# Optimization experiments

Hardware: AMD Instinct MI355X
Metric: run time of the kernel (lower is better)

## Reference

```python
import jax, jax.numpy as jnp
import numpy as np

HIDDEN = 4096
FFN = 14336
GS = 64  # groupsize


def dequant2(qw, scales, zeros, N):
    """Unpack 2-bit HQQ weights. qw: (N//4, K) int32, scales/zeros: (G, K).
    Returns W of shape (N, K) float: (bits - zeros[n % G]) * scales[n % G]."""
    G = scales.shape[0]
    n = jnp.arange(N)
    packed = qw[n // 4]                      # (N, K)
    shift = ((3 - (n % 4)) * 2).astype(qw.dtype)  # per-row bit shift
    vals = (packed >> shift[:, None]) & 3    # (N, K) 2-bit codes
    g = n % G
    return (vals.astype(scales.dtype) - zeros[g]) * scales[g]


def setup_inputs() -> dict:
    key = jax.random.key(0)
    ks = jax.random.split(key, 12)
    x = jax.random.normal(ks[0], (512, HIDDEN), dtype=jnp.float32)
    qw1 = jax.random.randint(ks[1], (FFN // 4, HIDDEN), 0, 256, dtype=jnp.int32)
    qw3 = jax.random.randint(ks[2], (FFN // 4, HIDDEN), 0, 256, dtype=jnp.int32)
    qw2 = jax.random.randint(ks[3], (HIDDEN // 4, FFN), 0, 256, dtype=jnp.int32)
    G1 = FFN // GS
    G2 = HIDDEN // GS
    s1 = jax.random.uniform(ks[4], (G1, HIDDEN), dtype=jnp.float32) * 0.05
    z1 = jax.random.uniform(ks[5], (G1, HIDDEN), dtype=jnp.float32)
    s3 = jax.random.uniform(ks[6], (G1, HIDDEN), dtype=jnp.float32) * 0.05
    z3 = jax.random.uniform(ks[7], (G1, HIDDEN), dtype=jnp.float32)
    s2 = jax.random.uniform(ks[8], (G2, FFN), dtype=jnp.float32) * 0.05
    z2 = jax.random.uniform(ks[9], (G2, FFN), dtype=jnp.float32)
    return {"x": x, "qw1": qw1, "s1": s1, "z1": z1, "qw3": qw3, "s3": s3,
            "z3": z3, "qw2": qw2, "s2": s2, "z2": z2, "groupsize": GS}


def reference(x, qw1, s1, z1, qw3, s3, z3, qw2, s2, z2, groupsize):
    # gate / up projections: C = x @ W^T, W dequantized to (N, K)
    w1 = dequant2(qw1, s1, z1, FFN)      # (FFN, HIDDEN)
    w3 = dequant2(qw3, s3, z3, FFN)      # (FFN, HIDDEN)
    w2 = dequant2(qw2, s2, z2, HIDDEN)   # (HIDDEN, FFN)
    gate = jnp.einsum('mk,nk->mn', x, w1)   # (M, FFN)
    up = jnp.einsum('mk,nk->mn', x, w3)     # (M, FFN)
    h = jax.nn.silu(gate) * up               # SwiGLU
    out = jnp.einsum('mf,hf->mh', h, w2)     # (M, HIDDEN)
    return out
```

## Files before the change

### kernel.cpp

```cpp
#include <hip/hip_runtime.h>
#include <hip/hip_fp16.h>
#include <stdint.h>

#define HIDDEN 4096
#define FFN    14336
#define MDIM   512
#define G1     224
#define G2     64
#define BK     64
#define KB_H   128
#define KB_F   448

typedef _Float16 f16x8 __attribute__((ext_vector_type(8)));
typedef float f32x4 __attribute__((ext_vector_type(4)));

#define SCHED0() __builtin_amdgcn_sched_barrier(0);
#define LGKM_BAR()                                            \
    asm volatile("s_waitcnt lgkmcnt(0)" ::: "memory");        \
    __builtin_amdgcn_s_barrier();                             \
    __builtin_amdgcn_sched_barrier(0);


__global__ void cvt_xp_kernel(const float* __restrict__ x, ushort* __restrict__ xbp) {
    int i = blockIdx.x * blockDim.x + threadIdx.x;
    int ls = i & 63;
    int kb = (i >> 6) & (KB_H - 1);
    int mb = i >> 13;
    int row = mb * 16 + (ls & 15);
    int col = kb * 32 + (ls >> 4) * 8;
    const float4* src = (const float4*)&x[(size_t)row * HIDDEN + col];
    float4 v0 = src[0], v1 = src[1];
    __half2 h0 = __floats2half2_rn(v0.x, v0.y);
    __half2 h1 = __floats2half2_rn(v0.z, v0.w);
    __half2 h2 = __floats2half2_rn(v1.x, v1.y);
    __half2 h3 = __floats2half2_rn(v1.z, v1.w);
    uint4 o = make_uint4(__builtin_bit_cast(uint32_t, h0), __builtin_bit_cast(uint32_t, h1),
                         __builtin_bit_cast(uint32_t, h2), __builtin_bit_cast(uint32_t, h3));
    ((uint4*)xbp)[i] = o;
}

__global__ void build_sz_kernel(const float* __restrict__ s, const float* __restrict__ z,
                                uint32_t* __restrict__ outp) {
    int i = blockIdx.x * blockDim.x + threadIdx.x;
    float s0 = s[2 * i], s1 = s[2 * i + 1];
    float z0 = z[2 * i], z1 = z[2 * i + 1];
    __half2 hs = __floats2half2_rn(s0, s1);
    __half2 hn = __floats2half2_rn(-z0 * s0, -z1 * s1);
    ((uint2*)outp)[i] = make_uint2(__builtin_bit_cast(uint32_t, hs),
                                   __builtin_bit_cast(uint32_t, hn));
}

__device__ __forceinline__ uint32_t deq2(uint32_t w0, uint32_t w1, uint32_t sh,
                                         uint32_t spair, uint32_t npair) {
    uint32_t c0 = (w0 >> sh) & 3u;
    uint32_t c1 = (w1 >> sh) & 3u;
    uint32_t sel = 0x01000100u + c0 * 0x0202u + c1 * 0x02020000u;
    uint32_t codes = __builtin_amdgcn_perm(0x42004000u, 0x3C000000u, sel);
    __half2 r = __hfma2(__builtin_bit_cast(__half2, codes),
                        __builtin_bit_cast(__half2, spair),
                        __builtin_bit_cast(__half2, npair));
    return __builtin_bit_cast(uint32_t, r);
}


__global__ __launch_bounds__(256, 3)
void gemm_gateup(const ushort* __restrict__ xbp, const uint32_t* __restrict__ qw1,
                 const uint32_t* __restrict__ sz1, const uint32_t* __restrict__ qw3,
                 const uint32_t* __restrict__ sz3, ushort* __restrict__ hp) {
    __shared__ ushort sB1[2][32 * 64];
    __shared__ ushort sB2[2][32 * 64];
    __shared__ ushort sE[256 * 32];

    const int tid = threadIdx.x;
    const int idx = ((blockIdx.x & 7) * 112) + (blockIdx.x >> 3);
    const int mt = idx & 1, nt = idx >> 1;
    const int m0 = mt * 256, n0 = nt * 32;

    const int lane = tid & 63, w = tid >> 6;
    const int wm = w * 64;
    const int frow = lane & 15, fk = (lane >> 4) * 8;
    const int sw = (frow & 7) << 3;

    uint32_t abase[4];
#pragma unroll
    for (int mi = 0; mi < 4; ++mi)
        abase[mi] = (uint32_t)(((m0 >> 4) + w * 4 + mi) * KB_H) * 512 + lane * 8;

    const int bi = tid & 127;
    const int rp = bi >> 3;
    const int kc = (bi & 7) * 8;
    const int row0 = rp * 2;
    const int g0 = (n0 + row0) % G1;
    const uint32_t* qp = (tid < 128 ? qw1 : qw3) + (size_t)(n0 / 4 + (rp >> 1)) * HIDDEN + kc;
    const uint32_t* zp = (tid < 128 ? sz1 : sz3) + (size_t)g0 * HIDDEN + kc;
    ushort (*sB)[32 * 64] = (tid < 128) ? sB1 : sB2;
    const uint32_t sh0 = 6u - 4u * (uint32_t)(rp & 1);
    const int wc0 = row0 * 64 + (kc ^ ((row0 & 7) << 3));
    const int wc1 = (row0 + 1) * 64 + (kc ^ (((row0 + 1) & 7) << 3));

    f32x4 accG[4][2], accU[4][2];
#pragma unroll
    for (int i = 0; i < 4; ++i)
#pragma unroll
        for (int j = 0; j < 2; ++j) {
            accG[i][j] = (f32x4){0.f, 0.f, 0.f, 0.f};
            accU[i][j] = (f32x4){0.f, 0.f, 0.f, 0.f};
        }

    f16x8 afE[4], afO[4];
    uint4 pw0, pw1, pz0, pz1, pz2, pz3;

#define GU_LDAE(tt)                                                            \
    { _Pragma("unroll")                                                        \
      for (int mi = 0; mi < 4; ++mi)                                           \
          afE[mi] = *(const f16x8*)&xbp[abase[mi] + (uint32_t)((tt) * 2) * 512]; }

#define GU_LDAO(tt)                                                            \
    { _Pragma("unroll")                                                        \
      for (int mi = 0; mi < 4; ++mi)                                           \
          afO[mi] = *(const f16x8*)&xbp[abase[mi] + (uint32_t)((tt) * 2 + 1) * 512]; }

#define GU_LDQZ(k0q)                                                           \
    pw0 = *(const uint4*)(qp + (k0q));                                         \
    pw1 = *(const uint4*)(qp + (k0q) + 4);                                     \
    pz0 = *(const uint4*)(zp + (k0q));                                         \
    pz1 = *(const uint4*)(zp + (k0q) + 4);                                     \
    pz2 = *(const uint4*)(zp + HIDDEN + (k0q));                                \
    pz3 = *(const uint4*)(zp + HIDDEN + (k0q) + 4);

#define GU_DEQ(wbuf)                                                           \
    { const uint32_t wv[8] = {pw0.x, pw0.y, pw0.z, pw0.w,                      \
                              pw1.x, pw1.y, pw1.z, pw1.w};                     \
      {   const uint32_t sp[4] = {pz0.x, pz0.z, pz1.x, pz1.z};                 \
          const uint32_t np[4] = {pz0.y, pz0.w, pz1.y, pz1.w};                 \
          uint32_t o[4];                                                       \
          _Pragma("unroll")                                                    \
          for (int j = 0; j < 4; ++j)                                          \
              o[j] = deq2(wv[2*j], wv[2*j+1], sh0, sp[j], np[j]);              \
          *(uint4*)&sB[wbuf][wc0] = make_uint4(o[0], o[1], o[2], o[3]);        \
      }                                                                        \
      {   const uint32_t sp[4] = {pz2.x, pz2.z, pz3.x, pz3.z};                 \
          const uint32_t np[4] = {pz2.y, pz2.w, pz3.y, pz3.w};                 \
          uint32_t o[4];                                                       \
          _Pragma("unroll")                                                    \
          for (int j = 0; j < 4; ++j)                                          \
              o[j] = deq2(wv[2*j], wv[2*j+1], sh0 - 2u, sp[j], np[j]);         \
          *(uint4*)&sB[wbuf][wc1] = make_uint4(o[0], o[1], o[2], o[3]);        \
      } }

#define GU_MFMA(AF, rbuf, kk)                                                  \
    { const int col = ((kk) * 32 + fk) ^ sw;                                   \
      f16x8 bg0 = *(const f16x8*)&sB1[rbuf][frow * 64 + col];                  \
      f16x8 bg1 = *(const f16x8*)&sB1[rbuf][(16 + frow) * 64 + col];           \
      f16x8 bu0 = *(const f16x8*)&sB2[rbuf][frow * 64 + col];                  \
      f16x8 bu1 = *(const f16x8*)&sB2[rbuf][(16 + frow) * 64 + col];           \
      __builtin_amdgcn_s_setprio(1);                                           \
      _Pragma("unroll")                                                        \
      for (int mi = 0; mi < 4; ++mi) {                                         \
          accG[mi][0] = __builtin_amdgcn_mfma_f32_16x16x32_f16(AF[mi], bg0, accG[mi][0], 0, 0, 0); \
          accG[mi][1] = __builtin_amdgcn_mfma_f32_16x16x32_f16(AF[mi], bg1, accG[mi][1], 0, 0, 0); \
          accU[mi][0] = __builtin_amdgcn_mfma_f32_16x16x32_f16(AF[mi], bu0, accU[mi][0], 0, 0, 0); \
          accU[mi][1] = __builtin_amdgcn_mfma_f32_16x16x32_f16(AF[mi], bu1, accU[mi][1], 0, 0, 0); \
      }                                                                        \
      __builtin_amdgcn_s_setprio(0); }

    GU_LDQZ(0)
    GU_LDAE(0)
    GU_LDAO(0)
    GU_DEQ(0)
    GU_LDQZ(BK)
    LGKM_BAR()

    for (int t = 0; t < 63; ++t) {
        GU_DEQ((t + 1) & 1)
        if (t < 62) { GU_LDQZ((t + 2) * BK) }
        GU_MFMA(afE, t & 1, 0)
        GU_LDAE(t + 1)
        GU_MFMA(afO, t & 1, 1)
        GU_LDAO(t + 1)
        LGKM_BAR()
    }
    GU_MFMA(afE, 1, 0)
    GU_MFMA(afO, 1, 1)

    const int rb = (lane >> 4) * 4, cb = lane & 15;
#pragma unroll
    for (int mi = 0; mi < 4; ++mi)
#pragma unroll
        for (int ni = 0; ni < 2; ++ni) {
            f32x4 g = accG[mi][ni], u = accU[mi][ni];
            const int row = wm + mi * 16 + rb;
            const int colx = ni * 16 + cb;
#pragma unroll
            for (int r = 0; r < 4; ++r) {
                float gv = g[r];
                float hv = __fdividef(gv, 1.0f + __expf(-gv)) * u[r];
                __half hh = __float2half(hv);
                sE[(row + r) * 32 + colx] = __builtin_bit_cast(ushort, hh);
            }
        }
    __syncthreads();
    {
#pragma unroll
        for (int j = 0; j < 4; ++j) {
            const int slot = tid + j * 256;
            const int mbi = slot >> 6, ls = slot & 63;
            uint4 v = *(const uint4*)&sE[(mbi * 16 + (ls & 15)) * 32 + (ls >> 4) * 8];
            *(uint4*)&hp[(size_t)(((m0 >> 4) + mbi) * KB_F + nt) * 512 + ls * 8] = v;
        }
    }
#undef GU_LDAE
#undef GU_LDAO
#undef GU_LDQZ
#undef GU_DEQ
#undef GU_MFMA
}


__global__ __launch_bounds__(256, 4)
void gemm_down(const ushort* __restrict__ hp, const uint32_t* __restrict__ qw2,
               const uint32_t* __restrict__ sz2, float* __restrict__ part) {
    __shared__ ushort sBd[2][32 * 64];

    const int tid = threadIdx.x;
    const int idx = ((blockIdx.x & 7) * 128) + (blockIdx.x >> 3);
    const int mt = idx & 3, nt = (idx >> 2) & 127, sk = idx >> 9;
    const int m0 = mt * 128, n0 = nt * 32;
    const int kb0 = sk * 224;
    const int kbeg = sk * (FFN / 2);

    const int lane = tid & 63, w = tid >> 6;
    const int wm = w * 32;
    const int frow = lane & 15, fk = (lane >> 4) * 8;
    const int sw = (frow & 7) << 3;

    uint32_t abase[2];
#pragma unroll
    for (int mi = 0; mi < 2; ++mi)
        abase[mi] = (uint32_t)(((m0 >> 4) + w * 2 + mi) * KB_F + kb0) * 512 + lane * 8;

    const int r = tid >> 3;
    const int kc = (tid & 7) * 8;
    const int g = ((nt & 1) * 32) + r;
    const uint32_t* qp = qw2 + (size_t)(n0 / 4 + (r >> 2)) * FFN + kbeg + kc;
    const uint32_t* zp = sz2 + (size_t)g * FFN + kbeg + kc;
    const uint32_t sh = 6u - 2u * (uint32_t)(r & 3);
    const int wc = r * 64 + (kc ^ ((r & 7) << 3));

    f32x4 acc[2][2];
#pragma unroll
    for (int i = 0; i < 2; ++i)
#pragma unroll
        for (int j = 0; j < 2; ++j) acc[i][j] = (f32x4){0.f, 0.f, 0.f, 0.f};

    f16x8 afE[2], afO[2];
    uint4 pw0, pw1, pz0, pz1;

#define GD_LDAE(tt)                                                            \
    { _Pragma("unroll")                                                        \
      for (int mi = 0; mi < 2; ++mi)                                           \
          afE[mi] = *(const f16x8*)&hp[abase[mi] + (uint32_t)((tt) * 2) * 512]; }

#define GD_LDAO(tt)                                                            \
    { _Pragma("unroll")                                                        \
      for (int mi = 0; mi < 2; ++mi)                                           \
          afO[mi] = *(const f16x8*)&hp[abase[mi] + (uint32_t)((tt) * 2 + 1) * 512]; }

#define GD_LDQZ(k0q)                                                           \
    pw0 = *(const uint4*)(qp + (k0q));                                         \
    pw1 = *(const uint4*)(qp + (k0q) + 4);                                     \
    pz0 = *(const uint4*)(zp + (k0q));                                         \
    pz1 = *(const uint4*)(zp + (k0q) + 4);

#define GD_DEQ(wbuf)                                                           \
    { const uint32_t wv[8] = {pw0.x, pw0.y, pw0.z, pw0.w,                      \
                              pw1.x, pw1.y, pw1.z, pw1.w};                     \
      const uint32_t sp[4] = {pz0.x, pz0.z, pz1.x, pz1.z};                     \
      const uint32_t np[4] = {pz0.y, pz0.w, pz1.y, pz1.w};                     \
      uint32_t o[4];                                                           \
      _Pragma("unroll")                                                        \
      for (int j = 0; j < 4; ++j)                                              \
          o[j] = deq2(wv[2*j], wv[2*j+1], sh, sp[j], np[j]);                   \
      *(uint4*)&sBd[wbuf][wc] = make_uint4(o[0], o[1], o[2], o[3]); }

#define GD_MFMA(AF, rbuf, kk)                                                  \
    { const int col = ((kk) * 32 + fk) ^ sw;                                   \
      f16x8 bf0 = *(const f16x8*)&sBd[rbuf][frow * 64 + col];                  \
      f16x8 bf1 = *(const f16x8*)&sBd[rbuf][(16 + frow) * 64 + col];           \
      __builtin_amdgcn_s_setprio(1);                                           \
      _Pragma("unroll")                                                        \
      for (int mi = 0; mi < 2; ++mi) {                                         \
          acc[mi][0] = __builtin_amdgcn_mfma_f32_16x16x32_f16(AF[mi], bf0, acc[mi][0], 0, 0, 0); \
          acc[mi][1] = __builtin_amdgcn_mfma_f32_16x16x32_f16(AF[mi], bf1, acc[mi][1], 0, 0, 0); \
      }                                                                        \
      __builtin_amdgcn_s_setprio(0); }

    GD_LDQZ(0)
    GD_LDAE(0)
    GD_LDAO(0)
    GD_DEQ(0)
    GD_LDQZ(BK)
    LGKM_BAR()

    for (int t = 0; t < 111; ++t) {
        GD_DEQ((t + 1) & 1)
        if (t < 110) { GD_LDQZ((t + 2) * BK) }
        GD_MFMA(afE, t & 1, 0)
        GD_LDAE(t + 1)
        GD_MFMA(afO, t & 1, 1)
        GD_LDAO(t + 1)
        LGKM_BAR()
    }
    GD_MFMA(afE, 1, 0)
    GD_MFMA(afO, 1, 1)

    float* pp = part + (size_t)sk * MDIM * HIDDEN;
    const int rb = (lane >> 4) * 4, cb = lane & 15;
#pragma unroll
    for (int mi = 0; mi < 2; ++mi)
#pragma unroll
        for (int ni = 0; ni < 2; ++ni) {
            f32x4 a = acc[mi][ni];
            const int mm = m0 + wm + mi * 16 + rb;
            const int nn = n0 + ni * 16 + cb;
#pragma unroll
            for (int rr = 0; rr < 4; ++rr) pp[(size_t)(mm + rr) * HIDDEN + nn] = a[rr];
        }
#undef GD_LDAE
#undef GD_LDAO
#undef GD_LDQZ
#undef GD_DEQ
#undef GD_MFMA
}


__global__ void reduce_out(const float* __restrict__ part, float* __restrict__ out) {
    int i = blockIdx.x * blockDim.x + threadIdx.x;
    const int Q = MDIM * HIDDEN / 4;
    float4 a = ((const float4*)part)[i];
    float4 b = ((const float4*)part)[i + Q];
    float4 o;
    o.x = a.x + b.x; o.y = a.y + b.y; o.z = a.z + b.z; o.w = a.w + b.w;
    ((float4*)out)[i] = o;
}


extern "C" void kernel_launch(void* const* d_in, const int* in_sizes, int n_in,
                              void* d_out, int out_size, void* d_ws, size_t ws_size,
                              hipStream_t stream) {
    (void)in_sizes; (void)n_in; (void)out_size; (void)ws_size;

    const float* x  = (const float*)d_in[0];
    const uint32_t* qw1 = (const uint32_t*)d_in[1];
    const float* s1 = (const float*)d_in[2];
    const float* z1 = (const float*)d_in[3];
    const uint32_t* qw3 = (const uint32_t*)d_in[4];
    const float* s3 = (const float*)d_in[5];
    const float* z3 = (const float*)d_in[6];
    const uint32_t* qw2 = (const uint32_t*)d_in[7];
    const float* s2 = (const float*)d_in[8];
    const float* z2 = (const float*)d_in[9];
    float* out = (float*)d_out;

    char* ws = (char*)d_ws;
    ushort*   xbp  = (ushort*)ws;
    uint32_t* szp1 = (uint32_t*)(ws + (size_t)MDIM * HIDDEN * 2);
    uint32_t* szp3 = szp1 + (size_t)G1 * HIDDEN;
    uint32_t* szp2 = szp3 + (size_t)G1 * HIDDEN;
    ushort*   hp   = (ushort*)(szp2 + (size_t)G2 * FFN);
    float*    part = (float*)((char*)hp + (size_t)MDIM * FFN * 2);

    cvt_xp_kernel<<<(MDIM * HIDDEN / 8) / 256, 256, 0, stream>>>(x, xbp);
    build_sz_kernel<<<(G1 * HIDDEN / 2) / 256, 256, 0, stream>>>(s1, z1, szp1);
    build_sz_kernel<<<(G1 * HIDDEN / 2) / 256, 256, 0, stream>>>(s3, z3, szp3);
    build_sz_kernel<<<(G2 * FFN / 2) / 256, 256, 0, stream>>>(s2, z2, szp2);

    gemm_gateup<<<(FFN / 32) * (MDIM / 256), 256, 0, stream>>>(xbp, qw1, szp1, qw3, szp3, hp);
    gemm_down<<<2 * (MDIM / 128) * (HIDDEN / 32), 256, 0, stream>>>(hp, qw2, szp2, part);
    reduce_out<<<(MDIM * HIDDEN / 4) / 256, 256, 0, stream>>>(part, out);
}
```

Baseline: 329.7 us.

## Process two K-steps per barrier with 4-stage LDS buffers; enlarge down-proj M tile

Both GEMM kernels now dequantize and prefetch two K-steps of packed weights per iteration into a four-slot LDS ring. This halves the number of barriers and doubles the outstanding global loads per wave. The down-projection tile grows from 128 to 256 rows per block, which halves its grid and doubles weight reuse per dequantization. Both kernels now target 2 blocks per SM instead of 3 or 4, so they rely on more registers and LDS at lower occupancy.

```diff
diff --git a/kernel.cpp b/kernel.cpp
--- a/kernel.cpp
+++ b/kernel.cpp
@@ -63,12 +63,12 @@
 }
 
 
-__global__ __launch_bounds__(256, 3)
+__global__ __launch_bounds__(256, 2)
 void gemm_gateup(const ushort* __restrict__ xbp, const uint32_t* __restrict__ qw1,
                  const uint32_t* __restrict__ sz1, const uint32_t* __restrict__ qw3,
                  const uint32_t* __restrict__ sz3, ushort* __restrict__ hp) {
-    __shared__ ushort sB1[2][32 * 64];
-    __shared__ ushort sB2[2][32 * 64];
+    __shared__ ushort sB1[4][32 * 64];
+    __shared__ ushort sB2[4][32 * 64];
     __shared__ ushort sE[256 * 32];
 
     const int tid = threadIdx.x;
@@ -108,7 +108,8 @@
         }
 
     f16x8 afE[4], afO[4];
-    uint4 pw0, pw1, pz0, pz1, pz2, pz3;
+    uint4 pwE0, pwE1, pzE0, pzE1, pzE2, pzE3;
+    uint4 pwO0, pwO1, pzO0, pzO1, pzO2, pzO3;
 
 #define GU_LDAE(tt)                                                            \
     { _Pragma("unroll")                                                        \
@@ -120,27 +121,27 @@
       for (int mi = 0; mi < 4; ++mi)                                           \
           afO[mi] = *(const f16x8*)&xbp[abase[mi] + (uint32_t)((tt) * 2 + 1) * 512]; }
 
-#define GU_LDQZ(k0q)                                                           \
-    pw0 = *(const uint4*)(qp + (k0q));                                         \
-    pw1 = *(const uint4*)(qp + (k0q) + 4);                                     \
-    pz0 = *(const uint4*)(zp + (k0q));                                         \
-    pz1 = *(const uint4*)(zp + (k0q) + 4);                                     \
-    pz2 = *(const uint4*)(zp + HIDDEN + (k0q));                                \
-    pz3 = *(const uint4*)(zp + HIDDEN + (k0q) + 4);
-
-#define GU_DEQ(wbuf)                                                           \
-    { const uint32_t wv[8] = {pw0.x, pw0.y, pw0.z, pw0.w,                      \
-                              pw1.x, pw1.y, pw1.z, pw1.w};                     \
-      {   const uint32_t sp[4] = {pz0.x, pz0.z, pz1.x, pz1.z};                 \
-          const uint32_t np[4] = {pz0.y, pz0.w, pz1.y, pz1.w};                 \
+#define GU_LDQZ(PW0, PW1, PZ0, PZ1, PZ2, PZ3, k0q)                             \
+    PW0 = *(const uint4*)(qp + (k0q));                                         \
+    PW1 = *(const uint4*)(qp + (k0q) + 4);                                     \
+    PZ0 = *(const uint4*)(zp + (k0q));                                         \
+    PZ1 = *(const uint4*)(zp + (k0q) + 4);                                     \
+    PZ2 = *(const uint4*)(zp + HIDDEN + (k0q));                                \
+    PZ3 = *(const uint4*)(zp + HIDDEN + (k0q) + 4);
+
+#define GU_DEQ(wbuf, PW0, PW1, PZ0, PZ1, PZ2, PZ3)                             \
+    { const uint32_t wv[8] = {(PW0).x, (PW0).y, (PW0).z, (PW0).w,              \
+                              (PW1).x, (PW1).y, (PW1).z, (PW1).w};             \
+      {   const uint32_t sp[4] = {(PZ0).x, (PZ0).z, (PZ1).x, (PZ1).z};         \
+          const uint32_t np[4] = {(PZ0).y, (PZ0).w, (PZ1).y, (PZ1).w};         \
           uint32_t o[4];                                                       \
           _Pragma("unroll")                                                    \
           for (int j = 0; j < 4; ++j)                                          \
               o[j] = deq2(wv[2*j], wv[2*j+1], sh0, sp[j], np[j]);              \
           *(uint4*)&sB[wbuf][wc0] = make_uint4(o[0], o[1], o[2], o[3]);        \
       }                                                                        \
-      {   const uint32_t sp[4] = {pz2.x, pz2.z, pz3.x, pz3.z};                 \
-          const uint32_t np[4] = {pz2.y, pz2.w, pz3.y, pz3.w};                 \
+      {   const uint32_t sp[4] = {(PZ2).x, (PZ2).z, (PZ3).x, (PZ3).z};         \
+          const uint32_t np[4] = {(PZ2).y, (PZ2).w, (PZ3).y, (PZ3).w};         \
           uint32_t o[4];                                                       \
           _Pragma("unroll")                                                    \
           for (int j = 0; j < 4; ++j)                                          \
@@ -164,24 +165,40 @@
       }                                                                        \
       __builtin_amdgcn_s_setprio(0); }
 
-    GU_LDQZ(0)
+#define GU_COMPT(rbuf, tnext)                                                  \
+    { GU_MFMA(afE, rbuf, 0)                                                    \
+      GU_LDAE(tnext)                                                           \
+      GU_MFMA(afO, rbuf, 1)                                                    \
+      GU_LDAO(tnext) }
+
+    GU_LDQZ(pwE0, pwE1, pzE0, pzE1, pzE2, pzE3, 0)
+    GU_LDQZ(pwO0, pwO1, pzO0, pzO1, pzO2, pzO3, BK)
     GU_LDAE(0)
     GU_LDAO(0)
-    GU_DEQ(0)
-    GU_LDQZ(BK)
+    GU_DEQ(0, pwE0, pwE1, pzE0, pzE1, pzE2, pzE3)
+    GU_DEQ(1, pwO0, pwO1, pzO0, pzO1, pzO2, pzO3)
+    GU_LDQZ(pwE0, pwE1, pzE0, pzE1, pzE2, pzE3, 2 * BK)
+    GU_LDQZ(pwO0, pwO1, pzO0, pzO1, pzO2, pzO3, 3 * BK)
     LGKM_BAR()
 
-    for (int t = 0; t < 63; ++t) {
-        GU_DEQ((t + 1) & 1)
-        if (t < 62) { GU_LDQZ((t + 2) * BK) }
-        GU_MFMA(afE, t & 1, 0)
-        GU_LDAE(t + 1)
-        GU_MFMA(afO, t & 1, 1)
-        GU_LDAO(t + 1)
+    for (int ww = 0; ww < 31; ++ww) {
+        const int rb0 = 2 * (ww & 1);
+        const int wb0 = 2 * ((ww + 1) & 1);
+        GU_DEQ(wb0,     pwE0, pwE1, pzE0, pzE1, pzE2, pzE3)
+        GU_DEQ(wb0 + 1, pwO0, pwO1, pzO0, pzO1, pzO2, pzO3)
+        SCHED0()
+        if (ww < 30) {
+            GU_LDQZ(pwE0, pwE1, pzE0, pzE1, pzE2, pzE3, (2 * ww + 4) * BK)
+            GU_LDQZ(pwO0, pwO1, pzO0, pzO1, pzO2, pzO3, (2 * ww + 5) * BK)
+        }
+        SCHED0()
+        GU_COMPT(rb0,     2 * ww + 1)
+        GU_COMPT(rb0 + 1, 2 * ww + 2)
         LGKM_BAR()
     }
-    GU_MFMA(afE, 1, 0)
-    GU_MFMA(afO, 1, 1)
+    GU_COMPT(2, 63)
+    GU_MFMA(afE, 3, 0)
+    GU_MFMA(afO, 3, 1)
 
     const int rb = (lane >> 4) * 4, cb = lane & 15;
 #pragma unroll
@@ -214,30 +231,31 @@
 #undef GU_LDQZ
 #undef GU_DEQ
 #undef GU_MFMA
-}
-
-
-__global__ __launch_bounds__(256, 4)
+#undef GU_COMPT
+}
+
+
+__global__ __launch_bounds__(256, 2)
 void gemm_down(const ushort* __restrict__ hp, const uint32_t* __restrict__ qw2,
                const uint32_t* __restrict__ sz2, float* __restrict__ part) {
-    __shared__ ushort sBd[2][32 * 64];
+    __shared__ ushort sBd[4][32 * 64];
 
     const int tid = threadIdx.x;
-    const int idx = ((blockIdx.x & 7) * 128) + (blockIdx.x >> 3);
-    const int mt = idx & 3, nt = (idx >> 2) & 127, sk = idx >> 9;
-    const int m0 = mt * 128, n0 = nt * 32;
+    const int idx = ((blockIdx.x & 7) * 64) + (blockIdx.x >> 3);
+    const int mt = idx & 1, nt = (idx >> 1) & 127, sk = idx >> 8;
+    const int m0 = mt * 256, n0 = nt * 32;
     const int kb0 = sk * 224;
     const int kbeg = sk * (FFN / 2);
 
     const int lane = tid & 63, w = tid >> 6;
-    const int wm = w * 32;
+    const int wm = w * 64;
     const int frow = lane & 15, fk = (lane >> 4) * 8;
     const int sw = (frow & 7) << 3;
 
-    uint32_t abase[2];
-#pragma unroll
-    for (int mi = 0; mi < 2; ++mi)
-        abase[mi] = (uint32_t)(((m0 >> 4) + w * 2 + mi) * KB_F + kb0) * 512 + lane * 8;
+    uint32_t abase[4];
+#pragma unroll
+    for (int mi = 0; mi < 4; ++mi)
+        abase[mi] = (uint32_t)(((m0 >> 4) + w * 4 + mi) * KB_F + kb0) * 512 + lane * 8;
 
     const int r = tid >> 3;
     const int kc = (tid & 7) * 8;
@@ -247,36 +265,37 @@
     const uint32_t sh = 6u - 2u * (uint32_t)(r & 3);
     const int wc = r * 64 + (kc ^ ((r & 7) << 3));
 
-    f32x4 acc[2][2];
-#pragma unroll
-    for (int i = 0; i < 2; ++i)
+    f32x4 acc[4][2];
+#pragma unroll
+    for (int i = 0; i < 4; ++i)
 #pragma unroll
         for (int j = 0; j < 2; ++j) acc[i][j] = (f32x4){0.f, 0.f, 0.f, 0.f};
 
-    f16x8 afE[2], afO[2];
-    uint4 pw0, pw1, pz0, pz1;
+    f16x8 afE[4], afO[4];
+    uint4 pwE0, pwE1, pzE0, pzE1;
+    uint4 pwO0, pwO1, pzO0, pzO1;
 
 #define GD_LDAE(tt)                                                            \
     { _Pragma("unroll")                                                        \
-      for (int mi = 0; mi < 2; ++mi)                                           \
+      for (int mi = 0; mi < 4; ++mi)                                           \
           afE[mi] = *(const f16x8*)&hp[abase[mi] + (uint32_t)((tt) * 2) * 512]; }
 
 #define GD_LDAO(tt)                                                            \
     { _Pragma("unroll")                                                        \
-      for (int mi = 0; mi < 2; ++mi)                                           \
+      for (int mi = 0; mi < 4; ++mi)                                           \
           afO[mi] = *(const f16x8*)&hp[abase[mi] + (uint32_t)((tt) * 2 + 1) * 512]; }
 
-#define GD_LDQZ(k0q)                                                           \
-    pw0 = *(const uint4*)(qp + (k0q));                                         \
-    pw1 = *(const uint4*)(qp + (k0q) + 4);                                     \
-    pz0 = *(const uint4*)(zp + (k0q));                                         \
-    pz1 = *(const uint4*)(zp + (k0q) + 4);
-
-#define GD_DEQ(wbuf)                                                           \
-    { const uint32_t wv[8] = {pw0.x, pw0.y, pw0.z, pw0.w,                      \
-                              pw1.x, pw1.y, pw1.z, pw1.w};                     \
-      const uint32_t sp[4] = {pz0.x, pz0.z, pz1.x, pz1.z};                     \
-      const uint32_t np[4] = {pz0.y, pz0.w, pz1.y, pz1.w};                     \
+#define GD_LDQZ(PW0, PW1, PZ0, PZ1, k0q)                                       \
+    PW0 = *(const uint4*)(qp + (k0q));                                         \
+    PW1 = *(const uint4*)(qp + (k0q) + 4);                                     \
+    PZ0 = *(const uint4*)(zp + (k0q));                                         \
+    PZ1 = *(const uint4*)(zp + (k0q) + 4);
+
+#define GD_DEQ(wbuf, PW0, PW1, PZ0, PZ1)                                       \
+    { const uint32_t wv[8] = {(PW0).x, (PW0).y, (PW0).z, (PW0).w,              \
+                              (PW1).x, (PW1).y, (PW1).z, (PW1).w};             \
+      const uint32_t sp[4] = {(PZ0).x, (PZ0).z, (PZ1).x, (PZ1).z};             \
+      const uint32_t np[4] = {(PZ0).y, (PZ0).w, (PZ1).y, (PZ1).w};             \
       uint32_t o[4];                                                           \
       _Pragma("unroll")                                                        \
       for (int j = 0; j < 4; ++j)                                              \
@@ -289,35 +308,51 @@
       f16x8 bf1 = *(const f16x8*)&sBd[rbuf][(16 + frow) * 64 + col];           \
       __builtin_amdgcn_s_setprio(1);                                           \
       _Pragma("unroll")                                                        \
-      for (int mi = 0; mi < 2; ++mi) {                                         \
+      for (int mi = 0; mi < 4; ++mi) {                                         \
           acc[mi][0] = __builtin_amdgcn_mfma_f32_16x16x32_f16(AF[mi], bf0, acc[mi][0], 0, 0, 0); \
           acc[mi][1] = __builtin_amdgcn_mfma_f32_16x16x32_f16(AF[mi], bf1, acc[mi][1], 0, 0, 0); \
       }                                                                        \
       __builtin_amdgcn_s_setprio(0); }
 
-    GD_LDQZ(0)
+#define GD_COMPT(rbuf, tnext)                                                  \
+    { GD_MFMA(afE, rbuf, 0)                                                    \
+      GD_LDAE(tnext)                                                           \
+      GD_MFMA(afO, rbuf, 1)                                                    \
+      GD_LDAO(tnext) }
+
+    GD_LDQZ(pwE0, pwE1, pzE0, pzE1, 0)
+    GD_LDQZ(pwO0, pwO1, pzO0, pzO1, BK)
     GD_LDAE(0)
     GD_LDAO(0)
-    GD_DEQ(0)
-    GD_LDQZ(BK)
+    GD_DEQ(0, pwE0, pwE1, pzE0, pzE1)
+    GD_DEQ(1, pwO0, pwO1, pzO0, pzO1)
+    GD_LDQZ(pwE0, pwE1, pzE0, pzE1, 2 * BK)
+    GD_LDQZ(pwO0, pwO1, pzO0, pzO1, 3 * BK)
     LGKM_BAR()
 
-    for (int t = 0; t < 111; ++t) {
-        GD_DEQ((t + 1) & 1)
-        if (t < 110) { GD_LDQZ((t + 2) * BK) }
-        GD_MFMA(afE, t & 1, 0)
-        GD_LDAE(t + 1)
-        GD_MFMA(afO, t & 1, 1)
-        GD_LDAO(t + 1)
+    for (int ww = 0; ww < 55; ++ww) {
+        const int rb0 = 2 * (ww & 1);
+        const int wb0 = 2 * ((ww + 1) & 1);
+        GD_DEQ(wb0,     pwE0, pwE1, pzE0, pzE1)
+        GD_DEQ(wb0 + 1, pwO0, pwO1, pzO0, pzO1)
+        SCHED0()
+        if (ww < 54) {
+            GD_LDQZ(pwE0, pwE1, pzE0, pzE1, (2 * ww + 4) * BK)
+            GD_LDQZ(pwO0, pwO1, pzO0, pzO1, (2 * ww + 5) * BK)
+        }
+        SCHED0()
+        GD_COMPT(rb0,     2 * ww + 1)
+        GD_COMPT(rb0 + 1, 2 * ww + 2)
         LGKM_BAR()
     }
-    GD_MFMA(afE, 1, 0)
-    GD_MFMA(afO, 1, 1)
+    GD_COMPT(2, 111)
+    GD_MFMA(afE, 3, 0)
+    GD_MFMA(afO, 3, 1)
 
     float* pp = part + (size_t)sk * MDIM * HIDDEN;
     const int rb = (lane >> 4) * 4, cb = lane & 15;
 #pragma unroll
-    for (int mi = 0; mi < 2; ++mi)
+    for (int mi = 0; mi < 4; ++mi)
 #pragma unroll
         for (int ni = 0; ni < 2; ++ni) {
             f32x4 a = acc[mi][ni];
@@ -331,6 +366,7 @@
 #undef GD_LDQZ
 #undef GD_DEQ
 #undef GD_MFMA
+#undef GD_COMPT
 }
 
 
@@ -376,6 +412,6 @@
     build_sz_kernel<<<(G2 * FFN / 2) / 256, 256, 0, stream>>>(s2, z2, szp2);
 
     gemm_gateup<<<(FFN / 32) * (MDIM / 256), 256, 0, stream>>>(xbp, qw1, szp1, qw3, szp3, hp);
-    gemm_down<<<2 * (MDIM / 128) * (HIDDEN / 32), 256, 0, stream>>>(hp, qw2, szp2, part);
+    gemm_down<<<2 * (MDIM / 256) * (HIDDEN / 32), 256, 0, stream>>>(hp, qw2, szp2, part);
     reduce_out<<<(MDIM * HIDDEN / 4) / 256, 256, 0, stream>>>(part, out);
 }
```

Result: faster. 290.2 us (-12.0%).
